# Performance work log

Hardware: AMD Instinct MI355X
Metric: run time of the kernel (lower is better)

The kernel has to match this reference:

```python
import jax, jax.numpy as jnp
import numpy as np

E, D, DFF = 8, 1024, 4096

def setup_inputs() -> dict:
    key = jax.random.key(0)
    ks = jax.random.split(key, 10)
    s = 0.02
    return {
        "x":  jax.random.normal(ks[0], (4, 2048, D), dtype=jnp.float32),
        "Wr": jax.random.normal(ks[1], (D, E), dtype=jnp.float32) * s,
        "br": jnp.zeros((E,), dtype=jnp.float32),
        "W1": jax.random.normal(ks[2], (E, D, DFF), dtype=jnp.float32) * s,
        "b1": jnp.zeros((E, DFF), dtype=jnp.float32),
        "W2": jax.random.normal(ks[3], (E, D, DFF), dtype=jnp.float32) * s,
        "b2": jnp.zeros((E, DFF), dtype=jnp.float32),
        "W3": jax.random.normal(ks[4], (E, DFF, D), dtype=jnp.float32) * s,
        "b3": jnp.zeros((E, D), dtype=jnp.float32),
    }

def reference(x, Wr, br, W1, b1, W2, b2, W3, b3):
    b, s, d = x.shape
    xt = x.reshape(b * s, d)                       # [T, D]
    logits = xt @ Wr + br                          # [T, E]
    pr, idx = jax.lax.top_k(logits, 2)             # [T, 2]
    w = jax.nn.softmax(pr, axis=-1)                # softmax over the 2 selected experts
    # combine weight per (token, expert): sum of routing weights where expert selected
    onehot = jax.nn.one_hot(idx, W1.shape[0], dtype=x.dtype)  # [T, 2, E]
    cw = jnp.einsum('tk,tke->te', w, onehot)       # [T, E]
    y = jnp.zeros_like(xt)
    for e in range(W1.shape[0]):                   # small fixed expert loop
        h = jax.nn.silu(xt @ W1[e] + b1[e]) * (xt @ W2[e] + b2[e])  # SwiGLU [T, DFF]
        y = y + (h @ W3[e] + b3[e]) * cw[:, e:e + 1]
    return y.reshape(b, s, d)
```

## Files before the change

kernel.cpp:

```cpp
#include <hip/hip_runtime.h>

#define T_TOK 8192
#define DIM   1024
#define DFF_  4096
#define NE    8
#define MAXT  144

typedef float  f32x4 __attribute__((ext_vector_type(4)));
typedef __bf16 b16x8 __attribute__((ext_vector_type(8)));

__device__ __forceinline__ unsigned short f2bf(float f) {
  union { float f; unsigned int u; } v; v.f = f;
  unsigned int r = v.u + 0x7fffu + ((v.u >> 16) & 1u);
  return (unsigned short)(r >> 16);
}

__device__ __forceinline__ void gload_lds16(const void* g, void* l) {
  __builtin_amdgcn_global_load_lds((const __attribute__((address_space(1))) void*)g,
                                   (__attribute__((address_space(3))) void*)l,
                                   16, 0, 0);
}

#define DRAIN_VMCNT() asm volatile("s_waitcnt vmcnt(0)" ::: "memory")

__global__ __launch_bounds__(256) void transpose_cvt(const float* __restrict__ src,
                                                     unsigned short* __restrict__ dst,
                                                     int R, int C) {
  __shared__ float tile[64][65];
  size_t mat = (size_t)blockIdx.z * R * C;
  int c0 = blockIdx.x * 64, r0 = blockIdx.y * 64;
  int lc = threadIdx.x & 63, q = threadIdx.x >> 6;
  const float* s = src + mat + (size_t)r0 * C + c0;
#pragma unroll
  for (int i = 0; i < 16; i++) {
    int r = q + i * 4;
    tile[r][lc] = s[(size_t)r * C + lc];
  }
  __syncthreads();
  unsigned short* d = dst + mat + (size_t)c0 * R + r0;
  int lc2 = (threadIdx.x & 31) * 2, cq = threadIdx.x >> 5;
#pragma unroll
  for (int i = 0; i < 8; i++) {
    int cc = cq + i * 8;
    unsigned lo = f2bf(tile[lc2][cc]);
    unsigned hi = f2bf(tile[lc2 + 1][cc]);
    *(unsigned*)(&d[(size_t)cc * R + lc2]) = lo | (hi << 16);
  }
}

__global__ __launch_bounds__(256) void router_k(const float* __restrict__ x,
                                                const float* __restrict__ Wr,
                                                const float* __restrict__ br,
                                                unsigned short* __restrict__ Xbf,
                                                int* __restrict__ top2e,
                                                float* __restrict__ top2w,
                                                int* __restrict__ counts) {
  __shared__ int lcnt[NE];
  if (threadIdx.x < NE) lcnt[threadIdx.x] = 0;
  __syncthreads();
  int wid = threadIdx.x >> 6, lane = threadIdx.x & 63;
  int t = blockIdx.x * 4 + wid;
  const float* xr = x + (size_t)t * DIM;
  unsigned short* xb = Xbf + (size_t)t * DIM;
  float s[NE];
#pragma unroll
  for (int e = 0; e < NE; e++) s[e] = 0.f;
  for (int i = 0; i < DIM / 64; i++) {
    int dd = i * 64 + lane;
    float xv = xr[dd];
    xb[dd] = f2bf(xv);
    const float* w = Wr + (size_t)dd * NE;
#pragma unroll
    for (int e = 0; e < NE; e++) s[e] += xv * w[e];
  }
#pragma unroll
  for (int m = 32; m >= 1; m >>= 1) {
#pragma unroll
    for (int e = 0; e < NE; e++) s[e] += __shfl_xor(s[e], m, 64);
  }
  if (lane == 0) {
#pragma unroll
    for (int e = 0; e < NE; e++) s[e] += br[e];
    int e0 = 0;
#pragma unroll
    for (int e = 1; e < NE; e++) if (s[e] > s[e0]) e0 = e;
    int e1 = (e0 == 0) ? 1 : 0;
#pragma unroll
    for (int e = 0; e < NE; e++) if (e != e0 && s[e] > s[e1]) e1 = e;
    float w0 = 1.f / (1.f + expf(s[e1] - s[e0]));
    top2e[2 * t] = e0; top2e[2 * t + 1] = e1;
    top2w[2 * t] = w0; top2w[2 * t + 1] = 1.f - w0;
    atomicAdd(&lcnt[e0], 1);
    atomicAdd(&lcnt[e1], 1);
  }
  __syncthreads();
  if (threadIdx.x < NE) atomicAdd(&counts[threadIdx.x], lcnt[threadIdx.x]);
}

__global__ void scan_build(int* __restrict__ ctrl) {
  if (threadIdx.x != 0 || blockIdx.x != 0) return;
  int* counts = ctrl;
  int* offsets = ctrl + 8;
  int* cursors = ctrl + 16;
  int* ntile = ctrl + 24;
  int* tileE = ctrl + 32;
  int* tileM = ctrl + 32 + MAXT;
  int o = 0;
  for (int e = 0; e < NE; e++) { offsets[e] = o; cursors[e] = o; o += counts[e]; }
  int nt = 0;
  for (int e = 0; e < NE; e++)
    for (int m0 = 0; m0 < counts[e]; m0 += 128) { tileE[nt] = e; tileM[nt] = m0; nt++; }
  ntile[0] = nt;
}

__global__ __launch_bounds__(256) void scatter_k(const int* __restrict__ top2e,
                                                 const float* __restrict__ top2w,
                                                 int* __restrict__ cursors,
                                                 int* __restrict__ list_tok,
                                                 float* __restrict__ list_w) {
  __shared__ int lcnt[NE];
  __shared__ int lbase[NE];
  int tid = threadIdx.x;
  if (tid < NE) lcnt[tid] = 0;
  __syncthreads();
  int t = blockIdx.x * 256 + tid;
  int e0 = top2e[2 * t], e1 = top2e[2 * t + 1];
  int r0 = atomicAdd(&lcnt[e0], 1);
  int r1 = atomicAdd(&lcnt[e1], 1);
  __syncthreads();
  if (tid < NE) lbase[tid] = atomicAdd(&cursors[tid], lcnt[tid]);
  __syncthreads();
  int p0 = lbase[e0] + r0, p1 = lbase[e1] + r1;
  list_tok[p0] = t; list_w[p0] = top2w[2 * t];
  list_tok[p1] = t; list_w[p1] = top2w[2 * t + 1];
}

__global__ __launch_bounds__(512) void gemm1_k(const unsigned short* __restrict__ Xbf,
                                               const unsigned short* __restrict__ W1T,
                                               const unsigned short* __restrict__ W2T,
                                               const float* __restrict__ b1,
                                               const float* __restrict__ b2,
                                               unsigned short* __restrict__ H,
                                               const int* __restrict__ list_tok,
                                               const int* __restrict__ ctrl) {
  const int* counts = ctrl; const int* offsets = ctrl + 8;
  const int* ntile = ctrl + 24;
  const int* tileE = ctrl + 32; const int* tileM = ctrl + 32 + MAXT;
  int bt = blockIdx.y;
  if (bt >= ntile[0]) return;
  int e = tileE[bt], m0 = tileM[bt];
  int Me = counts[e], off = offsets[e];
  int n0 = blockIdx.x * 128;

  __shared__ unsigned short lds[2][3 * 128 * 32];

  int tid = threadIdx.x, lane = tid & 63, wid = tid >> 6;
  int wr = wid >> 2, wc = wid & 3;

  const unsigned short* gsrc[3];
  unsigned ldsoff[3];
  {
    int lr = lane >> 2;
    int sc = ((lane & 3) ^ ((lane >> 3) & 3)) * 8;
#pragma unroll
    for (int j = 0; j < 3; j++) {
      int c = wid * 3 + j;
      ldsoff[j] = c * 512;
      if (c < 8) {
        int r = c * 16 + lr;
        int tok = (m0 + r < Me) ? list_tok[off + m0 + r] : list_tok[off];
        gsrc[j] = Xbf + (size_t)tok * DIM + sc;
      } else if (c < 16) {
        int n = n0 + (c - 8) * 16 + lr;
        gsrc[j] = W1T + ((size_t)e * DFF_ + n) * DIM + sc;
      } else {
        int n = n0 + (c - 16) * 16 + lr;
        gsrc[j] = W2T + ((size_t)e * DFF_ + n) * DIM + sc;
      }
    }
  }

  unsigned aoff[4], boff[2];
  {
    int colg = lane >> 4;
#pragma unroll
    for (int fi = 0; fi < 4; fi++) {
      int row = wr * 64 + fi * 16 + (lane & 15);
      aoff[fi] = row * 32 + ((colg ^ ((row >> 1) & 3)) * 8);
    }
#pragma unroll
    for (int fj = 0; fj < 2; fj++) {
      int row = wc * 32 + fj * 16 + (lane & 15);
      boff[fj] = row * 32 + ((colg ^ ((row >> 1) & 3)) * 8);
    }
  }

  f32x4 acc1[4][2], acc2[4][2];
#pragma unroll
  for (int i = 0; i < 4; i++)
#pragma unroll
    for (int j = 0; j < 2; j++) {
      acc1[i][j] = f32x4{0.f, 0.f, 0.f, 0.f};
      acc2[i][j] = f32x4{0.f, 0.f, 0.f, 0.f};
    }

  auto compute = [&](const unsigned short* base) {
    const unsigned short* sA  = base;
    const unsigned short* sB1 = base + 4096;
    const unsigned short* sB2 = base + 8192;
    b16x8 aF[4], bF1[2], bF2[2];
#pragma unroll
    for (int fi = 0; fi < 4; fi++) aF[fi] = *(const b16x8*)(sA + aoff[fi]);
#pragma unroll
    for (int fj = 0; fj < 2; fj++) {
      bF1[fj] = *(const b16x8*)(sB1 + boff[fj]);
      bF2[fj] = *(const b16x8*)(sB2 + boff[fj]);
    }
#pragma unroll
    for (int fi = 0; fi < 4; fi++)
#pragma unroll
      for (int fj = 0; fj < 2; fj++) {
        acc1[fi][fj] = __builtin_amdgcn_mfma_f32_16x16x32_bf16(aF[fi], bF1[fj], acc1[fi][fj], 0, 0, 0);
        acc2[fi][fj] = __builtin_amdgcn_mfma_f32_16x16x32_bf16(aF[fi], bF2[fj], acc2[fi][fj], 0, 0, 0);
      }
  };

#pragma unroll
  for (int j = 0; j < 3; j++) gload_lds16(gsrc[j], (void*)(&lds[0][ldsoff[j]]));
  DRAIN_VMCNT();
  __syncthreads();

  int cur = 0;
  const int NK = DIM / 32;
  for (int kt = 0; kt < NK; kt++) {
    if (kt + 1 < NK) {
#pragma unroll
      for (int j = 0; j < 3; j++)
        gload_lds16(gsrc[j] + (kt + 1) * 32, (void*)(&lds[cur ^ 1][ldsoff[j]]));
    }
    compute(&lds[cur][0]);
    DRAIN_VMCNT();
    __syncthreads();
    cur ^= 1;
  }

#pragma unroll
  for (int fi = 0; fi < 4; fi++)
#pragma unroll
    for (int fj = 0; fj < 2; fj++) {
      int col = n0 + wc * 32 + fj * 16 + (lane & 15);
      float bb1 = b1[e * DFF_ + col], bb2 = b2[e * DFF_ + col];
      int rbase = wr * 64 + fi * 16 + (lane >> 4) * 4;
#pragma unroll
      for (int r = 0; r < 4; r++) {
        int rr = rbase + r;
        if (m0 + rr < Me) {
          float c1 = acc1[fi][fj][r] + bb1;
          float c2 = acc2[fi][fj][r] + bb2;
          float h = c1 * c2 / (1.f + __expf(-c1));
          H[(size_t)(off + m0 + rr) * DFF_ + col] = f2bf(h);
        }
      }
    }
}

__global__ __launch_bounds__(512) void gemm2_k(const unsigned short* __restrict__ H,
                                               const unsigned short* __restrict__ W3T,
                                               const float* __restrict__ b3,
                                               const int* __restrict__ list_tok,
                                               const float* __restrict__ list_w,
                                               float* __restrict__ y,
                                               const int* __restrict__ ctrl) {
  const int* counts = ctrl; const int* offsets = ctrl + 8;
  const int* ntile = ctrl + 24;
  const int* tileE = ctrl + 32; const int* tileM = ctrl + 32 + MAXT;
  int bt = blockIdx.y;
  if (bt >= ntile[0]) return;
  int e = tileE[bt], m0 = tileM[bt];
  int Me = counts[e], off = offsets[e];
  int n0 = blockIdx.x * 128;

  __shared__ unsigned short lds[2][2 * 128 * 64];

  int tid = threadIdx.x, lane = tid & 63, wid = tid >> 6;
  int wr = wid >> 2, wc = wid & 3;

  const unsigned short* gsrc[4];
  unsigned ldsoff[4];
  {
    int lr = lane >> 3;
    int sc = ((lane & 7) ^ (lane >> 3)) * 8;
#pragma unroll
    for (int j = 0; j < 4; j++) {
      int c = wid * 4 + j;
      ldsoff[j] = c * 512;
      if (c < 16) {
        int r = c * 8 + lr;
        int pos = (m0 + r < Me) ? (off + m0 + r) : off;
        gsrc[j] = H + (size_t)pos * DFF_ + sc;
      } else {
        int n = n0 + (c - 16) * 8 + lr;
        gsrc[j] = W3T + ((size_t)e * DIM + n) * DFF_ + sc;
      }
    }
  }

  unsigned aoff[2][4], boff[2][2];
  {
    int colg = lane >> 4;
#pragma unroll
    for (int kk = 0; kk < 2; kk++) {
#pragma unroll
      for (int fi = 0; fi < 4; fi++) {
        int row = wr * 64 + fi * 16 + (lane & 15);
        aoff[kk][fi] = row * 64 + (((kk * 4 + colg) ^ (row & 7)) * 8);
      }
#pragma unroll
      for (int fj = 0; fj < 2; fj++) {
        int row = wc * 32 + fj * 16 + (lane & 15);
        boff[kk][fj] = row * 64 + (((kk * 4 + colg) ^ (row & 7)) * 8);
      }
    }
  }

  f32x4 acc[4][2];
#pragma unroll
  for (int i = 0; i < 4; i++)
#pragma unroll
    for (int j = 0; j < 2; j++) acc[i][j] = f32x4{0.f, 0.f, 0.f, 0.f};

  auto compute = [&](const unsigned short* base) {
    const unsigned short* sA = base;
    const unsigned short* sB = base + 128 * 64;
#pragma unroll
    for (int kk = 0; kk < 2; kk++) {
      b16x8 aF[4], bF[2];
#pragma unroll
      for (int fi = 0; fi < 4; fi++) aF[fi] = *(const b16x8*)(sA + aoff[kk][fi]);
#pragma unroll
      for (int fj = 0; fj < 2; fj++) bF[fj] = *(const b16x8*)(sB + boff[kk][fj]);
#pragma unroll
      for (int fi = 0; fi < 4; fi++)
#pragma unroll
        for (int fj = 0; fj < 2; fj++)
          acc[fi][fj] = __builtin_amdgcn_mfma_f32_16x16x32_bf16(aF[fi], bF[fj], acc[fi][fj], 0, 0, 0);
    }
  };

#pragma unroll
  for (int j = 0; j < 4; j++) gload_lds16(gsrc[j], (void*)(&lds[0][ldsoff[j]]));
  DRAIN_VMCNT();
  __syncthreads();

  int cur = 0;
  const int NK = DFF_ / 64;
  for (int kt = 0; kt < NK; kt++) {
    if (kt + 1 < NK) {
#pragma unroll
      for (int j = 0; j < 4; j++)
        gload_lds16(gsrc[j] + (kt + 1) * 64, (void*)(&lds[cur ^ 1][ldsoff[j]]));
    }
    compute(&lds[cur][0]);
    DRAIN_VMCNT();
    __syncthreads();
    cur ^= 1;
  }

#pragma unroll
  for (int fi = 0; fi < 4; fi++)
#pragma unroll
    for (int fj = 0; fj < 2; fj++) {
      int col = n0 + wc * 32 + fj * 16 + (lane & 15);
      float bb3 = b3[e * DIM + col];
      int rbase = wr * 64 + fi * 16 + (lane >> 4) * 4;
#pragma unroll
      for (int r = 0; r < 4; r++) {
        int rr = rbase + r;
        if (m0 + rr < Me) {
          int pos = off + m0 + rr;
          float v = list_w[pos] * (acc[fi][fj][r] + bb3);
          atomicAdd(&y[(size_t)list_tok[pos] * DIM + col], v);
        }
      }
    }
}

extern "C" void kernel_launch(void* const* d_in, const int* in_sizes, int n_in,
                              void* d_out, int out_size, void* d_ws, size_t ws_size,
                              hipStream_t stream) {
  (void)in_sizes; (void)n_in; (void)ws_size;
  const float* x  = (const float*)d_in[0];
  const float* Wr = (const float*)d_in[1];
  const float* br = (const float*)d_in[2];
  const float* W1 = (const float*)d_in[3];
  const float* b1 = (const float*)d_in[4];
  const float* W2 = (const float*)d_in[5];
  const float* b2 = (const float*)d_in[6];
  const float* W3 = (const float*)d_in[7];
  const float* b3 = (const float*)d_in[8];
  float* y = (float*)d_out;
  char* ws = (char*)d_ws;

  const size_t matB = (size_t)NE * DFF_ * DIM * 2;
  size_t oW1T = 0;
  size_t oW2T = oW1T + matB;
  size_t oXbf = oW2T + matB;
  size_t oH   = oXbf + (size_t)T_TOK * DIM * 2;
  size_t oT2e = oH + (size_t)2 * T_TOK * DFF_ * 2;
  size_t oT2w = oT2e + (size_t)2 * T_TOK * 4;
  size_t oLtk = oT2w + (size_t)2 * T_TOK * 4;
  size_t oLw  = oLtk + (size_t)2 * T_TOK * 4;
  size_t oCtl = oLw + (size_t)2 * T_TOK * 4;

  unsigned short* W1T = (unsigned short*)(ws + oW1T);
  unsigned short* W2T = (unsigned short*)(ws + oW2T);
  unsigned short* W3T = (unsigned short*)(ws + oW1T);
  unsigned short* Xbf = (unsigned short*)(ws + oXbf);
  unsigned short* Hb  = (unsigned short*)(ws + oH);
  int*   top2e = (int*)(ws + oT2e);
  float* top2w = (float*)(ws + oT2w);
  int*   ltok  = (int*)(ws + oLtk);
  float* lw    = (float*)(ws + oLw);
  int*   ctrl  = (int*)(ws + oCtl);

  hipMemsetAsync(y, 0, (size_t)out_size * 4, stream);
  hipMemsetAsync(ctrl, 0, (32 + 2 * MAXT) * 4, stream);

  transpose_cvt<<<dim3(DFF_ / 64, DIM / 64, NE), 256, 0, stream>>>(W1, W1T, DIM, DFF_);
  transpose_cvt<<<dim3(DFF_ / 64, DIM / 64, NE), 256, 0, stream>>>(W2, W2T, DIM, DFF_);
  router_k<<<dim3(T_TOK / 4), 256, 0, stream>>>(x, Wr, br, Xbf, top2e, top2w, ctrl);
  scan_build<<<dim3(1), 64, 0, stream>>>(ctrl);
  scatter_k<<<dim3(T_TOK / 256), 256, 0, stream>>>(top2e, top2w, ctrl + 16, ltok, lw);
  gemm1_k<<<dim3(DFF_ / 128, MAXT - 8), 512, 0, stream>>>(Xbf, W1T, W2T, b1, b2, Hb, ltok, ctrl);
  transpose_cvt<<<dim3(DIM / 64, DFF_ / 64, NE), 256, 0, stream>>>(W3, W3T, DFF_, DIM);
  gemm2_k<<<dim3(DIM / 128, MAXT - 8), 512, 0, stream>>>(Hb, W3T, b3, ltok, lw, y, ctrl);
}
```

Baseline: 771.1 us.

## Retile gemm1 to 256-row tiles with 1024 threads and K=64, vectorize transpose

gemm1 now runs 1024-thread blocks over 256-token by 128-column tiles with a K step of 64 and swizzled LDS. This halves the number of times each W1/W2 tile is fetched per expert and halves the count of K-loop barriers. scan_build now emits two tile lists, a 256-row list for gemm1 and a 128-row list for gemm2, and gemm2 reads its own list. transpose_cvt switches to float4 loads and 4-wide bf16 stores to cut memory instructions. In exchange, gemm1 uses 128KB of LDS per block, wider blocks limit occupancy and register budget, and padding waste in partial tiles grows.

```diff
diff --git a/kernel.cpp b/kernel.cpp
--- a/kernel.cpp
+++ b/kernel.cpp
@@ -8,6 +8,7 @@
 
 typedef float  f32x4 __attribute__((ext_vector_type(4)));
 typedef __bf16 b16x8 __attribute__((ext_vector_type(8)));
+typedef unsigned short u16x4 __attribute__((ext_vector_type(4)));
 
 __device__ __forceinline__ unsigned short f2bf(float f) {
   union { float f; unsigned int u; } v; v.f = f;
@@ -26,25 +27,30 @@
 __global__ __launch_bounds__(256) void transpose_cvt(const float* __restrict__ src,
                                                      unsigned short* __restrict__ dst,
                                                      int R, int C) {
-  __shared__ float tile[64][65];
+  __shared__ float tile[64][68];
   size_t mat = (size_t)blockIdx.z * R * C;
   int c0 = blockIdx.x * 64, r0 = blockIdx.y * 64;
-  int lc = threadIdx.x & 63, q = threadIdx.x >> 6;
+  int t = threadIdx.x;
+  int rcol = (t & 15) * 4, rrow = t >> 4;
   const float* s = src + mat + (size_t)r0 * C + c0;
 #pragma unroll
-  for (int i = 0; i < 16; i++) {
-    int r = q + i * 4;
-    tile[r][lc] = s[(size_t)r * C + lc];
+  for (int i = 0; i < 4; i++) {
+    int r = rrow + i * 16;
+    f32x4 v = *(const f32x4*)(s + (size_t)r * C + rcol);
+    *(f32x4*)(&tile[r][rcol]) = v;
   }
   __syncthreads();
   unsigned short* d = dst + mat + (size_t)c0 * R + r0;
-  int lc2 = (threadIdx.x & 31) * 2, cq = threadIdx.x >> 5;
-#pragma unroll
-  for (int i = 0; i < 8; i++) {
-    int cc = cq + i * 8;
-    unsigned lo = f2bf(tile[lc2][cc]);
-    unsigned hi = f2bf(tile[lc2 + 1][cc]);
-    *(unsigned*)(&d[(size_t)cc * R + lc2]) = lo | (hi << 16);
+  int wrow4 = (t & 15) * 4, wcol = t >> 4;
+#pragma unroll
+  for (int i = 0; i < 4; i++) {
+    int cc = wcol + i * 16;
+    u16x4 o;
+    o[0] = f2bf(tile[wrow4 + 0][cc]);
+    o[1] = f2bf(tile[wrow4 + 1][cc]);
+    o[2] = f2bf(tile[wrow4 + 2][cc]);
+    o[3] = f2bf(tile[wrow4 + 3][cc]);
+    *(u16x4*)(&d[(size_t)cc * R + wrow4]) = o;
   }
 }
 
@@ -102,15 +108,21 @@
   int* counts = ctrl;
   int* offsets = ctrl + 8;
   int* cursors = ctrl + 16;
-  int* ntile = ctrl + 24;
-  int* tileE = ctrl + 32;
-  int* tileM = ctrl + 32 + MAXT;
+  int* nt256 = ctrl + 24;
+  int* nt128 = ctrl + 25;
+  int* tE256 = ctrl + 32;
+  int* tM256 = ctrl + 32 + MAXT;
+  int* tE128 = ctrl + 32 + 2 * MAXT;
+  int* tM128 = ctrl + 32 + 3 * MAXT;
   int o = 0;
   for (int e = 0; e < NE; e++) { offsets[e] = o; cursors[e] = o; o += counts[e]; }
-  int nt = 0;
-  for (int e = 0; e < NE; e++)
-    for (int m0 = 0; m0 < counts[e]; m0 += 128) { tileE[nt] = e; tileM[nt] = m0; nt++; }
-  ntile[0] = nt;
+  int a = 0, b = 0;
+  for (int e = 0; e < NE; e++) {
+    for (int m0 = 0; m0 < counts[e]; m0 += 256) { tE256[a] = e; tM256[a] = m0; a++; }
+    for (int m0 = 0; m0 < counts[e]; m0 += 128) { tE128[b] = e; tM128[b] = m0; b++; }
+  }
+  nt256[0] = a;
+  nt128[0] = b;
 }
 
 __global__ __launch_bounds__(256) void scatter_k(const int* __restrict__ top2e,
@@ -135,14 +147,14 @@
   list_tok[p1] = t; list_w[p1] = top2w[2 * t + 1];
 }
 
-__global__ __launch_bounds__(512) void gemm1_k(const unsigned short* __restrict__ Xbf,
-                                               const unsigned short* __restrict__ W1T,
-                                               const unsigned short* __restrict__ W2T,
-                                               const float* __restrict__ b1,
-                                               const float* __restrict__ b2,
-                                               unsigned short* __restrict__ H,
-                                               const int* __restrict__ list_tok,
-                                               const int* __restrict__ ctrl) {
+__global__ __launch_bounds__(1024, 4) void gemm1_k(const unsigned short* __restrict__ Xbf,
+                                                   const unsigned short* __restrict__ W1T,
+                                                   const unsigned short* __restrict__ W2T,
+                                                   const float* __restrict__ b1,
+                                                   const float* __restrict__ b2,
+                                                   unsigned short* __restrict__ H,
+                                                   const int* __restrict__ list_tok,
+                                                   const int* __restrict__ ctrl) {
   const int* counts = ctrl; const int* offsets = ctrl + 8;
   const int* ntile = ctrl + 24;
   const int* tileE = ctrl + 32; const int* tileM = ctrl + 32 + MAXT;
@@ -152,46 +164,49 @@
   int Me = counts[e], off = offsets[e];
   int n0 = blockIdx.x * 128;
 
-  __shared__ unsigned short lds[2][3 * 128 * 32];
+  __shared__ unsigned short lds[2][32768];
 
   int tid = threadIdx.x, lane = tid & 63, wid = tid >> 6;
   int wr = wid >> 2, wc = wid & 3;
 
-  const unsigned short* gsrc[3];
-  unsigned ldsoff[3];
+  const unsigned short* gsrc[4];
+  unsigned ldsoff[4];
   {
-    int lr = lane >> 2;
-    int sc = ((lane & 3) ^ ((lane >> 3) & 3)) * 8;
-#pragma unroll
-    for (int j = 0; j < 3; j++) {
-      int c = wid * 3 + j;
+    int lr = lane >> 3;
+    int sc = ((lane & 7) ^ (lane >> 3)) * 8;
+#pragma unroll
+    for (int j = 0; j < 4; j++) {
+      int c = wid * 4 + j;
       ldsoff[j] = c * 512;
-      if (c < 8) {
-        int r = c * 16 + lr;
+      if (c < 32) {
+        int r = c * 8 + lr;
         int tok = (m0 + r < Me) ? list_tok[off + m0 + r] : list_tok[off];
         gsrc[j] = Xbf + (size_t)tok * DIM + sc;
-      } else if (c < 16) {
-        int n = n0 + (c - 8) * 16 + lr;
+      } else if (c < 48) {
+        int n = n0 + (c - 32) * 8 + lr;
         gsrc[j] = W1T + ((size_t)e * DFF_ + n) * DIM + sc;
       } else {
-        int n = n0 + (c - 16) * 16 + lr;
+        int n = n0 + (c - 48) * 8 + lr;
         gsrc[j] = W2T + ((size_t)e * DFF_ + n) * DIM + sc;
       }
     }
   }
 
-  unsigned aoff[4], boff[2];
+  unsigned aoff[2][4], boff[2][2];
   {
     int colg = lane >> 4;
 #pragma unroll
-    for (int fi = 0; fi < 4; fi++) {
-      int row = wr * 64 + fi * 16 + (lane & 15);
-      aoff[fi] = row * 32 + ((colg ^ ((row >> 1) & 3)) * 8);
-    }
-#pragma unroll
-    for (int fj = 0; fj < 2; fj++) {
-      int row = wc * 32 + fj * 16 + (lane & 15);
-      boff[fj] = row * 32 + ((colg ^ ((row >> 1) & 3)) * 8);
+    for (int kk = 0; kk < 2; kk++) {
+#pragma unroll
+      for (int m = 0; m < 4; m++) {
+        int row = wr * 64 + m * 16 + (lane & 15);
+        aoff[kk][m] = row * 64 + (((kk * 4 + colg) ^ (row & 7)) * 8);
+      }
+#pragma unroll
+      for (int n = 0; n < 2; n++) {
+        int row = wc * 32 + n * 16 + (lane & 15);
+        boff[kk][n] = 16384 + row * 64 + (((kk * 4 + colg) ^ (row & 7)) * 8);
+      }
     }
   }
 
@@ -205,38 +220,38 @@
     }
 
   auto compute = [&](const unsigned short* base) {
-    const unsigned short* sA  = base;
-    const unsigned short* sB1 = base + 4096;
-    const unsigned short* sB2 = base + 8192;
-    b16x8 aF[4], bF1[2], bF2[2];
-#pragma unroll
-    for (int fi = 0; fi < 4; fi++) aF[fi] = *(const b16x8*)(sA + aoff[fi]);
-#pragma unroll
-    for (int fj = 0; fj < 2; fj++) {
-      bF1[fj] = *(const b16x8*)(sB1 + boff[fj]);
-      bF2[fj] = *(const b16x8*)(sB2 + boff[fj]);
-    }
-#pragma unroll
-    for (int fi = 0; fi < 4; fi++)
-#pragma unroll
-      for (int fj = 0; fj < 2; fj++) {
-        acc1[fi][fj] = __builtin_amdgcn_mfma_f32_16x16x32_bf16(aF[fi], bF1[fj], acc1[fi][fj], 0, 0, 0);
-        acc2[fi][fj] = __builtin_amdgcn_mfma_f32_16x16x32_bf16(aF[fi], bF2[fj], acc2[fi][fj], 0, 0, 0);
-      }
+#pragma unroll
+    for (int kk = 0; kk < 2; kk++) {
+      b16x8 aF[4], bF1[2], bF2[2];
+#pragma unroll
+      for (int m = 0; m < 4; m++) aF[m] = *(const b16x8*)(base + aoff[kk][m]);
+#pragma unroll
+      for (int n = 0; n < 2; n++) {
+        bF1[n] = *(const b16x8*)(base + boff[kk][n]);
+        bF2[n] = *(const b16x8*)(base + boff[kk][n] + 8192);
+      }
+#pragma unroll
+      for (int m = 0; m < 4; m++)
+#pragma unroll
+        for (int n = 0; n < 2; n++) {
+          acc1[m][n] = __builtin_amdgcn_mfma_f32_16x16x32_bf16(aF[m], bF1[n], acc1[m][n], 0, 0, 0);
+          acc2[m][n] = __builtin_amdgcn_mfma_f32_16x16x32_bf16(aF[m], bF2[n], acc2[m][n], 0, 0, 0);
+        }
+    }
   };
 
 #pragma unroll
-  for (int j = 0; j < 3; j++) gload_lds16(gsrc[j], (void*)(&lds[0][ldsoff[j]]));
+  for (int j = 0; j < 4; j++) gload_lds16(gsrc[j], (void*)(&lds[0][ldsoff[j]]));
   DRAIN_VMCNT();
   __syncthreads();
 
   int cur = 0;
-  const int NK = DIM / 32;
+  const int NK = DIM / 64;
   for (int kt = 0; kt < NK; kt++) {
     if (kt + 1 < NK) {
 #pragma unroll
-      for (int j = 0; j < 3; j++)
-        gload_lds16(gsrc[j] + (kt + 1) * 32, (void*)(&lds[cur ^ 1][ldsoff[j]]));
+      for (int j = 0; j < 4; j++)
+        gload_lds16(gsrc[j] + (kt + 1) * 64, (void*)(&lds[cur ^ 1][ldsoff[j]]));
     }
     compute(&lds[cur][0]);
     DRAIN_VMCNT();
@@ -245,23 +260,24 @@
   }
 
 #pragma unroll
-  for (int fi = 0; fi < 4; fi++)
-#pragma unroll
-    for (int fj = 0; fj < 2; fj++) {
-      int col = n0 + wc * 32 + fj * 16 + (lane & 15);
-      float bb1 = b1[e * DFF_ + col], bb2 = b2[e * DFF_ + col];
-      int rbase = wr * 64 + fi * 16 + (lane >> 4) * 4;
+  for (int n = 0; n < 2; n++) {
+    int col = n0 + wc * 32 + n * 16 + (lane & 15);
+    float bb1 = b1[e * DFF_ + col], bb2 = b2[e * DFF_ + col];
+#pragma unroll
+    for (int m = 0; m < 4; m++) {
+      int rbase = wr * 64 + m * 16 + (lane >> 4) * 4;
 #pragma unroll
       for (int r = 0; r < 4; r++) {
         int rr = rbase + r;
         if (m0 + rr < Me) {
-          float c1 = acc1[fi][fj][r] + bb1;
-          float c2 = acc2[fi][fj][r] + bb2;
+          float c1 = acc1[m][n][r] + bb1;
+          float c2 = acc2[m][n][r] + bb2;
           float h = c1 * c2 / (1.f + __expf(-c1));
           H[(size_t)(off + m0 + rr) * DFF_ + col] = f2bf(h);
         }
       }
     }
+  }
 }
 
 __global__ __launch_bounds__(512) void gemm2_k(const unsigned short* __restrict__ H,
@@ -272,8 +288,9 @@
                                                float* __restrict__ y,
                                                const int* __restrict__ ctrl) {
   const int* counts = ctrl; const int* offsets = ctrl + 8;
-  const int* ntile = ctrl + 24;
-  const int* tileE = ctrl + 32; const int* tileM = ctrl + 32 + MAXT;
+  const int* ntile = ctrl + 25;
+  const int* tileE = ctrl + 32 + 2 * MAXT;
+  const int* tileM = ctrl + 32 + 3 * MAXT;
   int bt = blockIdx.y;
   if (bt >= ntile[0]) return;
   int e = tileE[bt], m0 = tileM[bt];
@@ -318,7 +335,7 @@
 #pragma unroll
       for (int fj = 0; fj < 2; fj++) {
         int row = wc * 32 + fj * 16 + (lane & 15);
-        boff[kk][fj] = row * 64 + (((kk * 4 + colg) ^ (row & 7)) * 8);
+        boff[kk][fj] = 128 * 64 + row * 64 + (((kk * 4 + colg) ^ (row & 7)) * 8);
       }
     }
   }
@@ -330,15 +347,13 @@
     for (int j = 0; j < 2; j++) acc[i][j] = f32x4{0.f, 0.f, 0.f, 0.f};
 
   auto compute = [&](const unsigned short* base) {
-    const unsigned short* sA = base;
-    const unsigned short* sB = base + 128 * 64;
 #pragma unroll
     for (int kk = 0; kk < 2; kk++) {
       b16x8 aF[4], bF[2];
 #pragma unroll
-      for (int fi = 0; fi < 4; fi++) aF[fi] = *(const b16x8*)(sA + aoff[kk][fi]);
-#pragma unroll
-      for (int fj = 0; fj < 2; fj++) bF[fj] = *(const b16x8*)(sB + boff[kk][fj]);
+      for (int fi = 0; fi < 4; fi++) aF[fi] = *(const b16x8*)(base + aoff[kk][fi]);
+#pragma unroll
+      for (int fj = 0; fj < 2; fj++) bF[fj] = *(const b16x8*)(base + boff[kk][fj]);
 #pragma unroll
       for (int fi = 0; fi < 4; fi++)
 #pragma unroll
@@ -424,14 +439,14 @@
   int*   ctrl  = (int*)(ws + oCtl);
 
   hipMemsetAsync(y, 0, (size_t)out_size * 4, stream);
-  hipMemsetAsync(ctrl, 0, (32 + 2 * MAXT) * 4, stream);
+  hipMemsetAsync(ctrl, 0, (32 + 4 * MAXT) * 4, stream);
 
   transpose_cvt<<<dim3(DFF_ / 64, DIM / 64, NE), 256, 0, stream>>>(W1, W1T, DIM, DFF_);
   transpose_cvt<<<dim3(DFF_ / 64, DIM / 64, NE), 256, 0, stream>>>(W2, W2T, DIM, DFF_);
   router_k<<<dim3(T_TOK / 4), 256, 0, stream>>>(x, Wr, br, Xbf, top2e, top2w, ctrl);
   scan_build<<<dim3(1), 64, 0, stream>>>(ctrl);
   scatter_k<<<dim3(T_TOK / 256), 256, 0, stream>>>(top2e, top2w, ctrl + 16, ltok, lw);
-  gemm1_k<<<dim3(DFF_ / 128, MAXT - 8), 512, 0, stream>>>(Xbf, W1T, W2T, b1, b2, Hb, ltok, ctrl);
+  gemm1_k<<<dim3(DFF_ / 128, 71), 1024, 0, stream>>>(Xbf, W1T, W2T, b1, b2, Hb, ltok, ctrl);
   transpose_cvt<<<dim3(DIM / 64, DFF_ / 64, NE), 256, 0, stream>>>(W3, W3T, DFF_, DIM);
   gemm2_k<<<dim3(DIM / 128, MAXT - 8), 512, 0, stream>>>(Hb, W3T, b3, ltok, lw, y, ctrl);
 }
```

Measured after the change: 739.6 us. -4.1%, faster.
